# Optimization experiments

Hardware: AMD Instinct MI355X
Metric: run time of the kernel (lower is better)

The kernel has to match this reference:

```python
import jax, jax.numpy as jnp
import numpy as np

N_INPUT, NUM_CENTERS, DIM = 16384, 4096, 256


def setup_inputs() -> dict:
    key = jax.random.key(0)
    k1, k2, k3, k4 = jax.random.split(key, 4)
    x = jax.random.normal(k1, (N_INPUT, DIM), dtype=jnp.float32)
    centers = jax.random.normal(k2, (NUM_CENTERS, DIM), dtype=jnp.float32)
    # positive sigmas bounded away from 0 so exp(-d^2/2s^2) stays well-scaled
    sigmas = jax.random.uniform(k3, (NUM_CENTERS, DIM), dtype=jnp.float32) * 2.0 + 1.0
    w_lin = jax.random.normal(k4, (1, NUM_CENTERS), dtype=jnp.float32) * (1.0 / np.sqrt(NUM_CENTERS))
    b_lin = jnp.zeros((1,), dtype=jnp.float32)
    return {"x": x, "centers": centers, "sigmas": sigmas, "w_lin": w_lin, "b_lin": b_lin}


def reference(x, centers, sigmas, w_lin, b_lin):
    # Anisotropic squared Mahalanobis-style distance:
    #   d2[n,c] = sum_d (x[n,d]-centers[c,d])^2 / (2*sigmas[c,d]^2)
    # expanded into GEMMs to avoid the (n, c, d) intermediate.
    inv2s2 = 1.0 / (2.0 * sigmas * sigmas)                      # [C, D]
    d2 = (
        jnp.einsum("nd,cd->nc", x * x, inv2s2)                 # x^2 term
        - 2.0 * jnp.einsum("nd,cd->nc", x, centers * inv2s2)   # cross term
        + jnp.sum(centers * centers * inv2s2, axis=-1)          # c^2 term [C]
    )
    radial_val = jnp.exp(-d2)                                   # [N, C]
    class_score = radial_val @ w_lin.T + b_lin                  # [N, 1]
    return jax.nn.sigmoid(class_score)
```

## Files before the change

### kernel.cpp

```cpp
#include <hip/hip_runtime.h>
#include <cstdint>
#include <cstddef>

#define MDIM 16384
#define CDIM 4096
#define DDIM 256
#define KDIM 512
#define KB   256

typedef float f32x4  __attribute__((ext_vector_type(4)));
typedef int   i32x4v __attribute__((ext_vector_type(4)));
typedef int   i32x8v __attribute__((ext_vector_type(8)));

__device__ __forceinline__ unsigned q4(float v) {
    unsigned s = (__builtin_bit_cast(unsigned, v) >> 31) << 3;
    float a = fabsf(v);
    unsigned c = (unsigned)(a >= 0.25f) + (a >= 0.75f) + (a >= 1.25f)
               + (a >= 1.75f) + (a >= 2.5f) + (a >= 3.5f) + (a >= 5.0f);
    return s | c;
}
__device__ __forceinline__ unsigned pack8(const float* v) {
    unsigned w = 0;
    #pragma unroll
    for (int i = 0; i < 8; ++i) w |= q4(v[i]) << (4 * i);
    return w;
}

__global__ __launch_bounds__(256) void prep(
    const float* __restrict__ x, const float* __restrict__ centers,
    const float* __restrict__ sigmas,
    unsigned char* __restrict__ Ap, unsigned char* __restrict__ Bp,
    float* __restrict__ constc, float* __restrict__ score) {
    int b = blockIdx.x, tid = threadIdx.x;
    if (b < 2048) {
        int idx8 = b * 256 + tid;
        int n = idx8 >> 5, d8 = idx8 & 31;
        float v[8], v2[8];
        *(float4*)(v)     = ((const float4*)x)[idx8 * 2];
        *(float4*)(v + 4) = ((const float4*)x)[idx8 * 2 + 1];
        #pragma unroll
        for (int i = 0; i < 8; ++i) v2[i] = v[i] * v[i] * 0.125f;
        *(unsigned*)(Ap + (size_t)n * KB + d8 * 4)       = pack8(v);
        *(unsigned*)(Ap + (size_t)n * KB + 128 + d8 * 4) = pack8(v2);
        if (idx8 < MDIM) score[idx8] = 0.0f;
    } else {
        int gid8 = (b - 2048) * 256 + tid;
        int c = gid8 >> 5, d8 = gid8 & 31;
        float cv[8], sv[8], cr[8], iv[8];
        *(float4*)(cv)     = ((const float4*)centers)[gid8 * 2];
        *(float4*)(cv + 4) = ((const float4*)centers)[gid8 * 2 + 1];
        *(float4*)(sv)     = ((const float4*)sigmas)[gid8 * 2];
        *(float4*)(sv + 4) = ((const float4*)sigmas)[gid8 * 2 + 1];
        float t = 0.0f;
        #pragma unroll
        for (int i = 0; i < 8; ++i) {
            float inv = 1.0f / (2.0f * sv[i] * sv[i]);
            cr[i] = -2.0f * cv[i] * inv;
            iv[i] = inv * 8.0f;
            t += cv[i] * cv[i] * inv;
        }
        *(unsigned*)(Bp + (size_t)c * KB + d8 * 4)       = pack8(cr);
        *(unsigned*)(Bp + (size_t)c * KB + 128 + d8 * 4) = pack8(iv);
        #pragma unroll
        for (int m = 16; m; m >>= 1) t += __shfl_xor(t, m, 64);
        if ((tid & 31) == 0) constc[c] = t;
    }
}

__global__ __launch_bounds__(256, 4) void gemm_fused(
    const unsigned char* __restrict__ A, const unsigned char* __restrict__ B,
    const float* __restrict__ constc, const float* __restrict__ w,
    float* __restrict__ score) {

    __shared__ unsigned char As[128 * 128];
    __shared__ unsigned char Bs[128 * 128];

    const int tid  = threadIdx.x;
    const int wave = tid >> 6;
    const int lane = tid & 63;
    const int quad = lane >> 4;
    const int l16  = lane & 15;

    const int bm = blockIdx.y;
    const int bn = blockIdx.x;

    const int wave_m = wave * 32;

    f32x4 acc[2][8] = {};

    const int st_row = lane >> 3;
    const int st_k   = ((lane & 7) ^ st_row) * 16;

    const unsigned char* Abase = A + (size_t)(bm * 128) * KB;
    const unsigned char* Bbase = B + (size_t)(bn * 128) * KB;

    const int rsw = l16 & 7;

    #pragma unroll
    for (int k0 = 0; k0 < 2; ++k0) {
        const int sA = k0 ? 0x82828282 : 0x7F7F7F7F;
        const int sB = k0 ? 0x7C7C7C7C : 0x7F7F7F7F;
        #pragma unroll
        for (int c = 0; c < 4; ++c) {
            int slab = wave * 4 + c;
            const unsigned char* ga = Abase + (size_t)(slab * 8 + st_row) * KB + k0 * 128 + st_k;
            __builtin_amdgcn_global_load_lds(
                (const __attribute__((address_space(1))) void*)ga,
                (__attribute__((address_space(3))) void*)(As + slab * 1024), 16, 0, 0);
        }
        #pragma unroll
        for (int c = 0; c < 4; ++c) {
            int slab = wave * 4 + c;
            const unsigned char* gb = Bbase + (size_t)(slab * 8 + st_row) * KB + k0 * 128 + st_k;
            __builtin_amdgcn_global_load_lds(
                (const __attribute__((address_space(1))) void*)gb,
                (__attribute__((address_space(3))) void*)(Bs + slab * 1024), 16, 0, 0);
        }
        __syncthreads();

        #pragma unroll
        for (int kh = 0; kh < 2; ++kh) {
            const int sl = ((kh * 4 + quad) ^ rsw) * 16;
            i32x8v af[2];
            #pragma unroll
            for (int i = 0; i < 2; ++i) {
                i32x4v lo = *(const i32x4v*)(As + (wave_m + i * 16 + l16) * 128 + sl);
                af[i] = __builtin_shufflevector(lo, lo, 0, 1, 2, 3, -1, -1, -1, -1);
            }
            #pragma unroll
            for (int j = 0; j < 8; ++j) {
                i32x4v lo = *(const i32x4v*)(Bs + (j * 16 + l16) * 128 + sl);
                i32x8v bf = __builtin_shufflevector(lo, lo, 0, 1, 2, 3, -1, -1, -1, -1);
                #pragma unroll
                for (int i = 0; i < 2; ++i)
                    acc[i][j] = __builtin_amdgcn_mfma_scale_f32_16x16x128_f8f6f4(
                        af[i], bf, acc[i][j],
                        4 , 4 ,
                        0, sA, 0, sB);
            }
        }
        __syncthreads();
    }

    const float NEG_LOG2E = -1.4426950408889634f;
    float rowsum[2][4];
    #pragma unroll
    for (int i = 0; i < 2; ++i)
        #pragma unroll
        for (int r = 0; r < 4; ++r) rowsum[i][r] = 0.0f;

    #pragma unroll
    for (int j = 0; j < 8; ++j) {
        int ng = bn * 128 + j * 16 + l16;
        float wj  = w[ng];
        float cjl = NEG_LOG2E * constc[ng];
        #pragma unroll
        for (int i = 0; i < 2; ++i)
            #pragma unroll
            for (int r = 0; r < 4; ++r)
                rowsum[i][r] += exp2f(fmaf(acc[i][j][r], NEG_LOG2E, cjl)) * wj;
    }

    #pragma unroll
    for (int mask = 1; mask < 16; mask <<= 1)
        #pragma unroll
        for (int i = 0; i < 2; ++i)
            #pragma unroll
            for (int r = 0; r < 4; ++r)
                rowsum[i][r] += __shfl_xor(rowsum[i][r], mask, 64);

    if (l16 == 0) {
        #pragma unroll
        for (int i = 0; i < 2; ++i)
            #pragma unroll
            for (int r = 0; r < 4; ++r) {
                int mg = bm * 128 + wave_m + i * 16 + quad * 4 + r;
                atomicAdd(&score[mg], rowsum[i][r]);
            }
    }
}

__global__ void finalize(const float* __restrict__ score,
                         const float* __restrict__ b,
                         float* __restrict__ out) {
    int n = blockIdx.x * 256 + threadIdx.x;
    if (n < MDIM) {
        float s = score[n] + b[0];
        out[n] = 1.0f / (1.0f + exp2f(-1.4426950408889634f * s));
    }
}

extern "C" void kernel_launch(void* const* d_in, const int* in_sizes, int n_in,
                              void* d_out, int out_size, void* d_ws, size_t ws_size,
                              hipStream_t stream) {
    const float* x       = (const float*)d_in[0];
    const float* centers = (const float*)d_in[1];
    const float* sigmas  = (const float*)d_in[2];
    const float* w_lin   = (const float*)d_in[3];
    const float* b_lin   = (const float*)d_in[4];
    float* out = (float*)d_out;

    char* ws = (char*)d_ws;
    unsigned char* Ap = (unsigned char*)ws;
    unsigned char* Bp = (unsigned char*)(ws + (size_t)MDIM * KB);
    float* cc    = (float*)(ws + (size_t)MDIM * KB + (size_t)CDIM * KB);
    float* score = (float*)((char*)cc + CDIM * sizeof(float));

    prep<<<dim3(2048 + 512), dim3(256), 0, stream>>>(
        x, centers, sigmas, Ap, Bp, cc, score);
    gemm_fused<<<dim3(CDIM / 128, MDIM / 128), dim3(256), 0, stream>>>(
        Ap, Bp, cc, w_lin, score);
    finalize<<<dim3((MDIM + 255) / 256), dim3(256), 0, stream>>>(score, b_lin, out);
}
```

Baseline: 117.1 us.

## Load A fragments directly to registers and stage full-K B tile in LDS once

A operand fragments are now read straight from global memory into registers per wave instead of going through LDS. The whole 256-byte K extent of the B tile is staged into LDS in one pass, which removes the two-phase loop and one barrier. The goal is to cut LDS traffic and synchronisation. In exchange, A loads are uncoalesced per-lane 16-byte global reads, and with launch bounds lowered to 3 more registers are available but occupancy may drop.

Result: no change. 119.4 us (+1.9%).

```diff
diff --git a/kernel.cpp b/kernel.cpp
--- a/kernel.cpp
+++ b/kernel.cpp
@@ -67,13 +67,12 @@
     }
 }
 
-__global__ __launch_bounds__(256, 4) void gemm_fused(
+__global__ __launch_bounds__(256, 3) void gemm_fused(
     const unsigned char* __restrict__ A, const unsigned char* __restrict__ B,
     const float* __restrict__ constc, const float* __restrict__ w,
     float* __restrict__ score) {
 
-    __shared__ unsigned char As[128 * 128];
-    __shared__ unsigned char Bs[128 * 128];
+    __shared__ unsigned char Bs[128 * 256];
 
     const int tid  = threadIdx.x;
     const int wave = tid >> 6;
@@ -88,58 +87,54 @@
 
     f32x4 acc[2][8] = {};
 
-    const int st_row = lane >> 3;
-    const int st_k   = ((lane & 7) ^ st_row) * 16;
-
-    const unsigned char* Abase = A + (size_t)(bm * 128) * KB;
     const unsigned char* Bbase = B + (size_t)(bn * 128) * KB;
-
-    const int rsw = l16 & 7;
-
-    #pragma unroll
-    for (int k0 = 0; k0 < 2; ++k0) {
-        const int sA = k0 ? 0x82828282 : 0x7F7F7F7F;
-        const int sB = k0 ? 0x7C7C7C7C : 0x7F7F7F7F;
-        #pragma unroll
-        for (int c = 0; c < 4; ++c) {
-            int slab = wave * 4 + c;
-            const unsigned char* ga = Abase + (size_t)(slab * 8 + st_row) * KB + k0 * 128 + st_k;
-            __builtin_amdgcn_global_load_lds(
-                (const __attribute__((address_space(1))) void*)ga,
-                (__attribute__((address_space(3))) void*)(As + slab * 1024), 16, 0, 0);
-        }
-        #pragma unroll
-        for (int c = 0; c < 4; ++c) {
-            int slab = wave * 4 + c;
-            const unsigned char* gb = Bbase + (size_t)(slab * 8 + st_row) * KB + k0 * 128 + st_k;
+    {
+        const int rins = lane >> 4;
+        const int h    = (lane >> 3) & 1;
+        const int cst  = lane & 7;
+        #pragma unroll
+        for (int s8 = 0; s8 < 8; ++s8) {
+            int slab = wave * 8 + s8;
+            int row  = slab * 4 + rins;
+            const unsigned char* gb = Bbase + (size_t)row * KB + h * 128
+                                    + ((cst ^ (row & 7)) * 16);
             __builtin_amdgcn_global_load_lds(
                 (const __attribute__((address_space(1))) void*)gb,
                 (__attribute__((address_space(3))) void*)(Bs + slab * 1024), 16, 0, 0);
         }
-        __syncthreads();
-
-        #pragma unroll
-        for (int kh = 0; kh < 2; ++kh) {
-            const int sl = ((kh * 4 + quad) ^ rsw) * 16;
-            i32x8v af[2];
+    }
+
+    const unsigned char* Abase = A + (size_t)(bm * 128 + wave_m) * KB;
+    i32x4v af[2][4];
+    #pragma unroll
+    for (int i = 0; i < 2; ++i)
+        #pragma unroll
+        for (int kh = 0; kh < 4; ++kh)
+            af[i][kh] = *(const i32x4v*)(Abase + (size_t)(i * 16 + l16) * KB
+                                         + kh * 64 + quad * 16);
+
+    __syncthreads();
+
+    const int rsw = l16 & 7;
+    #pragma unroll
+    for (int kh = 0; kh < 4; ++kh) {
+        const int sA = (kh & 2) ? 0x82828282 : 0x7F7F7F7F;
+        const int sB = (kh & 2) ? 0x7C7C7C7C : 0x7F7F7F7F;
+        const int sl = (kh >> 1) * 128 + ((((kh & 1) * 4 + quad) ^ rsw) * 16);
+        #pragma unroll
+        for (int j = 0; j < 8; ++j) {
+            i32x4v lo = *(const i32x4v*)(Bs + (j * 16 + l16) * 256 + sl);
+            i32x8v bf = __builtin_shufflevector(lo, lo, 0, 1, 2, 3, -1, -1, -1, -1);
             #pragma unroll
             for (int i = 0; i < 2; ++i) {
-                i32x4v lo = *(const i32x4v*)(As + (wave_m + i * 16 + l16) * 128 + sl);
-                af[i] = __builtin_shufflevector(lo, lo, 0, 1, 2, 3, -1, -1, -1, -1);
-            }
-            #pragma unroll
-            for (int j = 0; j < 8; ++j) {
-                i32x4v lo = *(const i32x4v*)(Bs + (j * 16 + l16) * 128 + sl);
-                i32x8v bf = __builtin_shufflevector(lo, lo, 0, 1, 2, 3, -1, -1, -1, -1);
-                #pragma unroll
-                for (int i = 0; i < 2; ++i)
-                    acc[i][j] = __builtin_amdgcn_mfma_scale_f32_16x16x128_f8f6f4(
-                        af[i], bf, acc[i][j],
-                        4 , 4 ,
-                        0, sA, 0, sB);
+                i32x8v a8 = __builtin_shufflevector(af[i][kh], af[i][kh],
+                                                    0, 1, 2, 3, -1, -1, -1, -1);
+                acc[i][j] = __builtin_amdgcn_mfma_scale_f32_16x16x128_f8f6f4(
+                    a8, bf, acc[i][j],
+                    4 , 4 ,
+                    0, sA, 0, sB);
             }
         }
-        __syncthreads();
     }
 
     const float NEG_LOG2E = -1.4426950408889634f;
```
